# Kernel optimization log

Measured on AMD Instinct MI355X. Metric: run time of the kernel, lower is better.

## Reference

```python
import jax, jax.numpy as jnp
import numpy as np

N = 30000      # nodes
E = 480000     # edges (avg degree 16)
IN = 128       # atom in_channels
ED = 16        # edge_dim
D = 128        # hidden_channels
OUT = 64       # out_channels
L = 4          # num_layers + 1 GCNEConv layers


def setup_inputs() -> dict:
    key = jax.random.key(0)
    ks = jax.random.split(key, 8)
    w = lambda k, sh: (jax.random.normal(k, sh, dtype=jnp.float32) * 0.05)
    return {
        "x": jax.random.normal(ks[0], (N, IN), dtype=jnp.float32),
        "edge_index": jax.random.randint(ks[1], (2, E), 0, N, dtype=jnp.int64),
        "edge_attr": jax.random.normal(ks[2], (E, ED), dtype=jnp.float32),
        "W_atom": w(ks[3], (IN, D)), "b_atom": jnp.zeros((D,), jnp.float32),
        "W_bond": w(ks[4], (ED, D)), "b_bond": jnp.zeros((D,), jnp.float32),
        "W_seq": w(ks[5], (L, D, D)), "b_seq": jnp.zeros((L, D), jnp.float32),
        "W_lin": w(ks[6], (2 * D, OUT)), "b_lin": jnp.zeros((OUT,), jnp.float32),
    }


def _aggregate(h_bond, idx_i, n):
    # CMPNN 'message_booster': elementwise sum_agg * max_agg over incoming edges
    sum_agg = jax.ops.segment_sum(h_bond, idx_i, num_segments=n)
    max_agg = jax.ops.segment_max(h_bond, idx_i, num_segments=n)
    max_agg = jnp.where(jnp.isfinite(max_agg), max_agg, 0.0)  # empty segments -> 0
    return sum_agg * max_agg


def reference(x, edge_index, edge_attr, W_atom, b_atom, W_bond, b_bond,
              W_seq, b_seq, W_lin, b_lin):
    n = x.shape[0]
    idx_i = edge_index[0]  # flow='target_to_source' -> i is edge_index[0]
    idx_j = edge_index[1]

    x_proj = jax.nn.relu(x @ W_atom + b_atom)          # [N, D]
    h_atom = x_proj
    h_bond = jax.nn.relu(edge_attr @ W_bond + b_bond)  # [E, D]

    # first L-1 convs: node update + edge update
    for l in range(L - 1):
        msg = _aggregate(h_bond, idx_i, n)             # [N, D]
        h_atom = h_atom * msg                          # inner_product communicator
        # edge_update: x[edge_index_i] - edge_attr[edge_index_j] (node-index gather
        # into edge tensor, faithful to the original code; valid since E > N)
        bond = h_atom[idx_i] - h_bond[idx_j]           # [E, D]
        h_bond = jax.nn.relu(bond @ W_seq[l] + b_seq[l])

    # last conv: only the node output is used downstream
    msg = _aggregate(h_bond, idx_i, n)
    aggr_atom_message = h_atom * msg

    # top-level communicator (inner_product): hidden_state * message
    h_atom = h_atom * aggr_atom_message
    out = jnp.concatenate([h_atom, x_proj], axis=1) @ W_lin + b_lin  # [N, OUT]
    return out
```

## Files before the change

kernel.cpp:

```cpp
#include <hip/hip_runtime.h>
#include <hip/hip_bf16.h>

#define DD 128
#define SCB 256
#define CE  256

typedef __attribute__((ext_vector_type(8))) short bf16x8;
typedef __attribute__((ext_vector_type(4))) float f32x4;

__device__ __forceinline__ unsigned bf16_rne(float f) {
    unsigned u = __float_as_uint(f);
    return (u + 0x7fffu + ((u >> 16) & 1u)) >> 16;
}

__global__ __launch_bounds__(256)
void hist_kernel(const int* __restrict__ idx_i, int* __restrict__ cnt, int E)
{
    const int e = blockIdx.x * 256 + threadIdx.x;
    if (e < E) atomicAdd(&cnt[idx_i[e]], 1);
}

__global__ __launch_bounds__(SCB)
void scan1_kernel(const int* __restrict__ cnt, int* __restrict__ exc,
                  int* __restrict__ bsum, int n)
{
    __shared__ int s[SCB];
    const int i = blockIdx.x * SCB + (int)threadIdx.x;
    const int v = (i < n) ? cnt[i] : 0;
    s[threadIdx.x] = v;
    __syncthreads();
    #pragma unroll
    for (int off = 1; off < SCB; off <<= 1) {
        int t = (threadIdx.x >= off) ? s[threadIdx.x - off] : 0;
        __syncthreads();
        s[threadIdx.x] += t;
        __syncthreads();
    }
    if (i < n) exc[i] = s[threadIdx.x] - v;
    if (threadIdx.x == SCB - 1) bsum[blockIdx.x] = s[threadIdx.x];
}

__global__ __launch_bounds__(SCB)
void scan2_kernel(int* __restrict__ bsum, int nb)
{
    __shared__ int s[SCB];
    const int v = (threadIdx.x < nb) ? bsum[threadIdx.x] : 0;
    s[threadIdx.x] = v;
    __syncthreads();
    #pragma unroll
    for (int off = 1; off < SCB; off <<= 1) {
        int t = (threadIdx.x >= off) ? s[threadIdx.x - off] : 0;
        __syncthreads();
        s[threadIdx.x] += t;
        __syncthreads();
    }
    if (threadIdx.x < nb) bsum[threadIdx.x] = s[threadIdx.x] - v;
}

__global__ __launch_bounds__(SCB)
void scan3_kernel(int* __restrict__ exc, const int* __restrict__ bsum, int n)
{
    const int i = blockIdx.x * SCB + (int)threadIdx.x;
    if (i < n) exc[i] += bsum[i >> 8];
}

__global__ __launch_bounds__(256)
void scatter_kernel(const int* __restrict__ idx_i, const int* __restrict__ idx_j,
                    int* __restrict__ cursor, int* __restrict__ perm,
                    int* __restrict__ si, int* __restrict__ sj, int E)
{
    const int e = blockIdx.x * 256 + threadIdx.x;
    if (e < E) {
        const int n = idx_i[e];
        const int p = atomicAdd(&cursor[n], 1);
        perm[p] = e;
        si[p] = n;
        sj[p] = idx_j[e];
    }
}

__global__ __launch_bounds__(1024)
void gemm128_mfma_kernel(float* __restrict__ A0, const float* __restrict__ A1,
                         int nA, int nTotal,
                         const float* __restrict__ W, const float* __restrict__ bias,
                         int bias_limit, int do_relu, int update,
                         float* __restrict__ sum_agg, int* __restrict__ max_agg,
                         float* __restrict__ out0, float* __restrict__ out1,
                         int ntiles)
{
    __shared__ __align__(16) unsigned char SM[131584];
    char*  const Whi = (char*)SM;
    char*  const Wlo = (char*)SM + 32768;
    char*  const Ahi = (char*)SM + 65536;
    char*  const Alo = (char*)SM + 98304;
    float* const Wf  = (float*)(SM + 65536);
    float* const bs  = (float*)(SM + 131072);

    const int t = (int)threadIdx.x;

    {
        const float4* Wg = (const float4*)W;
        float4* Wd = (float4*)Wf;
        #pragma unroll
        for (int i = 0; i < 4; ++i) Wd[t + i * 1024] = Wg[t + i * 1024];
        if (t < DD) bs[t] = bias ? bias[t] : 0.f;
    }
    __syncthreads();
    {
        const int col = t >> 3;
        const int kb  = (t & 7) * 16;
        unsigned h16[16], l16[16];
        #pragma unroll
        for (int j = 0; j < 16; ++j) {
            const float w = Wf[(size_t)(kb + j) * DD + col];
            const unsigned hb = bf16_rne(w);
            const float hf = __uint_as_float(hb << 16);
            h16[j] = hb;
            l16[j] = bf16_rne(w - hf);
        }
        #pragma unroll
        for (int c = 0; c < 2; ++c) {
            uint4 ph, pl;
            ph.x = h16[c*8+0] | (h16[c*8+1] << 16);
            ph.y = h16[c*8+2] | (h16[c*8+3] << 16);
            ph.z = h16[c*8+4] | (h16[c*8+5] << 16);
            ph.w = h16[c*8+6] | (h16[c*8+7] << 16);
            pl.x = l16[c*8+0] | (l16[c*8+1] << 16);
            pl.y = l16[c*8+2] | (l16[c*8+3] << 16);
            pl.z = l16[c*8+4] | (l16[c*8+5] << 16);
            pl.w = l16[c*8+6] | (l16[c*8+7] << 16);
            const int off = ((col * 256 + (kb + c * 8) * 2)) ^ ((col & 7) << 4);
            *(uint4*)(Whi + off) = ph;
            *(uint4*)(Wlo + off) = pl;
        }
    }

    const int w  = t >> 6;
    const int l  = t & 63;
    const int wm = w >> 2;
    const int wn = w & 3;
    const int g  = l >> 4;
    const int q  = l & 15;

    for (int tile = blockIdx.x; tile < ntiles; tile += gridDim.x) {
        const int e0 = tile * 128;
        __syncthreads();

        #pragma unroll
        for (int i = 0; i < 2; ++i) {
            const int task = t + i * 1024;
            const int row  = task >> 4;
            const int c    = task & 15;
            const int rr = min(e0 + row, nTotal - 1);
            float d[8];
            if (rr < nA) {
                float* ph0 = A0 + (size_t)rr * DD + c * 8;
                const float4 a0 = *(const float4*)ph0;
                const float4 a1 = *(const float4*)(ph0 + 4);
                if (update) {
                    float* sp = sum_agg + (size_t)rr * DD + c * 8;
                    int*   mp = max_agg + (size_t)rr * DD + c * 8;
                    const float4 s0 = *(const float4*)sp;
                    const float4 s1 = *(const float4*)(sp + 4);
                    const int4   m0 = *(const int4*)mp;
                    const int4   m1 = *(const int4*)(mp + 4);
                    d[0] = a0.x * s0.x * __int_as_float(m0.x);
                    d[1] = a0.y * s0.y * __int_as_float(m0.y);
                    d[2] = a0.z * s0.z * __int_as_float(m0.z);
                    d[3] = a0.w * s0.w * __int_as_float(m0.w);
                    d[4] = a1.x * s1.x * __int_as_float(m1.x);
                    d[5] = a1.y * s1.y * __int_as_float(m1.y);
                    d[6] = a1.z * s1.z * __int_as_float(m1.z);
                    d[7] = a1.w * s1.w * __int_as_float(m1.w);
                    *(float4*)ph0       = make_float4(d[0], d[1], d[2], d[3]);
                    *(float4*)(ph0 + 4) = make_float4(d[4], d[5], d[6], d[7]);
                    *(float4*)sp       = make_float4(0.f, 0.f, 0.f, 0.f);
                    *(float4*)(sp + 4) = make_float4(0.f, 0.f, 0.f, 0.f);
                    *(int4*)mp       = make_int4(0, 0, 0, 0);
                    *(int4*)(mp + 4) = make_int4(0, 0, 0, 0);
                } else {
                    d[0] = a0.x; d[1] = a0.y; d[2] = a0.z; d[3] = a0.w;
                    d[4] = a1.x; d[5] = a1.y; d[6] = a1.z; d[7] = a1.w;
                }
            } else {
                const float* pa = A1 + (size_t)(rr - nA) * DD + c * 8;
                const float4 a0 = *(const float4*)pa;
                const float4 a1 = *(const float4*)(pa + 4);
                d[0] = a0.x; d[1] = a0.y; d[2] = a0.z; d[3] = a0.w;
                d[4] = a1.x; d[5] = a1.y; d[6] = a1.z; d[7] = a1.w;
            }
            unsigned h8[8], l8[8];
            #pragma unroll
            for (int j = 0; j < 8; ++j) {
                const unsigned hb = bf16_rne(d[j]);
                const float hf = __uint_as_float(hb << 16);
                h8[j] = hb;
                l8[j] = bf16_rne(d[j] - hf);
            }
            uint4 ph, pl;
            ph.x = h8[0] | (h8[1] << 16);
            ph.y = h8[2] | (h8[3] << 16);
            ph.z = h8[4] | (h8[5] << 16);
            ph.w = h8[6] | (h8[7] << 16);
            pl.x = l8[0] | (l8[1] << 16);
            pl.y = l8[2] | (l8[3] << 16);
            pl.z = l8[4] | (l8[5] << 16);
            pl.w = l8[6] | (l8[7] << 16);
            const int off = ((row * 256 + c * 16)) ^ ((row & 7) << 4);
            *(uint4*)(Ahi + off) = ph;
            *(uint4*)(Alo + off) = pl;
        }
        __syncthreads();

        f32x4 acc[2][2];
        const f32x4 zero = {0.f, 0.f, 0.f, 0.f};
        acc[0][0] = zero; acc[0][1] = zero; acc[1][0] = zero; acc[1][1] = zero;

        #pragma unroll
        for (int ks = 0; ks < 4; ++ks) {
            const int kbyte = ks * 64 + g * 16;
            bf16x8 ah[2], al[2], bh[2], bl[2];
            #pragma unroll
            for (int m = 0; m < 2; ++m) {
                const int row = wm * 32 + m * 16 + q;
                const int off = (row * 256 + kbyte) ^ ((row & 7) << 4);
                ah[m] = *(const bf16x8*)(Ahi + off);
                al[m] = *(const bf16x8*)(Alo + off);
            }
            #pragma unroll
            for (int n = 0; n < 2; ++n) {
                const int colv = wn * 32 + n * 16 + q;
                const int off = (colv * 256 + kbyte) ^ ((colv & 7) << 4);
                bh[n] = *(const bf16x8*)(Whi + off);
                bl[n] = *(const bf16x8*)(Wlo + off);
            }
            #pragma unroll
            for (int m = 0; m < 2; ++m)
                #pragma unroll
                for (int n = 0; n < 2; ++n)
                    acc[m][n] = __builtin_amdgcn_mfma_f32_16x16x32_bf16(ah[m], bh[n], acc[m][n], 0, 0, 0);
            #pragma unroll
            for (int m = 0; m < 2; ++m)
                #pragma unroll
                for (int n = 0; n < 2; ++n)
                    acc[m][n] = __builtin_amdgcn_mfma_f32_16x16x32_bf16(ah[m], bl[n], acc[m][n], 0, 0, 0);
            #pragma unroll
            for (int m = 0; m < 2; ++m)
                #pragma unroll
                for (int n = 0; n < 2; ++n)
                    acc[m][n] = __builtin_amdgcn_mfma_f32_16x16x32_bf16(al[m], bh[n], acc[m][n], 0, 0, 0);
        }

        #pragma unroll
        for (int n = 0; n < 2; ++n) {
            const int colv = wn * 32 + n * 16 + q;
            const float bv = bs[colv];
            #pragma unroll
            for (int m = 0; m < 2; ++m) {
                #pragma unroll
                for (int r = 0; r < 4; ++r) {
                    const int row = e0 + wm * 32 + m * 16 + g * 4 + r;
                    if (row < nTotal) {
                        float v = acc[m][n][r] + ((row < bias_limit) ? bv : 0.f);
                        if (do_relu) v = fmaxf(v, 0.f);
                        out0[(size_t)row * DD + colv] = v;
                        if (out1) out1[(size_t)row * DD + colv] = v;
                    }
                }
            }
        }
    }
}

__global__ __launch_bounds__(256)
void bond_proj_agg_kernel(const float* __restrict__ edge_attr,
                          const float* __restrict__ Wb, const float* __restrict__ bb,
                          const int* __restrict__ si, const int* __restrict__ perm,
                          float* __restrict__ h_head0,
                          float* __restrict__ sum_agg, int* __restrict__ max_agg,
                          int E, int N)
{
    __shared__ float Ws[16 * DD];
    __shared__ float bs2[DD];
    __shared__ __align__(16) float ea_s[32][16];
    __shared__ int ii2[32], pm2[32];

    for (int idx = (int)threadIdx.x; idx < 16 * DD; idx += 256) Ws[idx] = Wb[idx];
    if (threadIdx.x < DD) bs2[threadIdx.x] = bb[threadIdx.x];

    const int p0 = blockIdx.x * 32;
    {
        const int t = (int)threadIdx.x;
        const int row = t >> 3;
        const int k2 = (t & 7) * 2;
        const int ppc = min(p0 + row, E - 1);
        const int orig = perm[ppc];
        const float2 v2 = *(const float2*)(edge_attr + (size_t)orig * 16 + k2);
        ea_s[row][k2] = v2.x;
        ea_s[row][k2 + 1] = v2.y;
        if (t < 32) {
            const int q = min(p0 + t, E - 1);
            ii2[t] = si[q];
            pm2[t] = perm[q];
        }
    }
    __syncthreads();

    const int o    = threadIdx.x & 127;
    const int half = threadIdx.x >> 7;

    float wcol[16];
    #pragma unroll
    for (int k = 0; k < 16; ++k) wcol[k] = Ws[k * DD + o];
    const float bo = bs2[o];

    int curNode = ii2[half * 16];
    float rs = 0.f, rm = 0.f;
    #pragma unroll 4
    for (int j = 0; j < 16; ++j) {
        const int row = half * 16 + j;
        const float4* ear = (const float4*)(&ea_s[row][0]);
        const float4 q0 = ear[0], q1 = ear[1], q2 = ear[2], q3 = ear[3];
        float acc = bo;
        acc = fmaf(q0.x, wcol[ 0], acc);
        acc = fmaf(q0.y, wcol[ 1], acc);
        acc = fmaf(q0.z, wcol[ 2], acc);
        acc = fmaf(q0.w, wcol[ 3], acc);
        acc = fmaf(q1.x, wcol[ 4], acc);
        acc = fmaf(q1.y, wcol[ 5], acc);
        acc = fmaf(q1.z, wcol[ 6], acc);
        acc = fmaf(q1.w, wcol[ 7], acc);
        acc = fmaf(q2.x, wcol[ 8], acc);
        acc = fmaf(q2.y, wcol[ 9], acc);
        acc = fmaf(q2.z, wcol[10], acc);
        acc = fmaf(q2.w, wcol[11], acc);
        acc = fmaf(q3.x, wcol[12], acc);
        acc = fmaf(q3.y, wcol[13], acc);
        acc = fmaf(q3.z, wcol[14], acc);
        acc = fmaf(q3.w, wcol[15], acc);
        float v = fmaxf(acc, 0.f);
        const int pe = p0 + row;
        if (pe < E) {
            const int orig = pm2[row];
            if (orig < N) h_head0[(size_t)orig * DD + o] = v;
        } else {
            v = 0.f;
        }
        const int gi = ii2[row];
        if (gi != curNode) {
            atomicAdd(&sum_agg[(size_t)curNode * DD + o], rs);
            atomicMax(&max_agg[(size_t)curNode * DD + o], __float_as_int(rm));
            curNode = gi; rs = v; rm = v;
        } else {
            rs += v; rm = fmaxf(rm, v);
        }
    }
    atomicAdd(&sum_agg[(size_t)curNode * DD + o], rs);
    atomicMax(&max_agg[(size_t)curNode * DD + o], __float_as_int(rm));
}

__global__ __launch_bounds__(256)
void edge_pass_kernel(const float* __restrict__ PQ,
                      const int* __restrict__ si, const int* __restrict__ sj,
                      const int* __restrict__ perm,
                      float* __restrict__ head_next, int store_head,
                      float* __restrict__ sum_agg, int* __restrict__ max_agg,
                      int E, int N)
{
    __shared__ int si_s[CE], sj_s[CE], pm_s[CE];
    const int p0b = blockIdx.x * CE;
    if (p0b >= E) return;
    const int t = (int)threadIdx.x;
    {
        const int p = min(p0b + t, E - 1);
        si_s[t] = si[p];
        sj_s[t] = sj[p];
        pm_s[t] = perm[p];
    }
    __syncthreads();

    const int w    = t >> 6;
    const int lane = t & 63;
    const int c    = lane * 2;
    const int q0   = w * 64;
    const int pg0  = p0b + q0;
    if (pg0 >= E) return;

    const float* __restrict__ Qbase = PQ + (size_t)N * DD + c;

    float2 qa = *(const float2*)(Qbase + (size_t)sj_s[q0 + 0] * DD);
    float2 qb = *(const float2*)(Qbase + (size_t)sj_s[q0 + 1] * DD);
    float2 qc = *(const float2*)(Qbase + (size_t)sj_s[q0 + 2] * DD);
    float2 qd = *(const float2*)(Qbase + (size_t)sj_s[q0 + 3] * DD);

    int curNode = si_s[q0];
    float2 Pi = *(const float2*)(PQ + (size_t)curNode * DD + c);
    float2 rs = make_float2(0.f, 0.f), rm = make_float2(0.f, 0.f);

    #define EP_STEP(K, QREG)                                                     \
    {                                                                            \
        const int kk = (K);                                                      \
        const int i = si_s[q0 + kk];                                             \
        if (i != curNode) {                                                      \
            atomicAdd(&sum_agg[(size_t)curNode * DD + c],     rs.x);             \
            atomicAdd(&sum_agg[(size_t)curNode * DD + c + 1], rs.y);             \
            atomicMax(&max_agg[(size_t)curNode * DD + c],     __float_as_int(rm.x)); \
            atomicMax(&max_agg[(size_t)curNode * DD + c + 1], __float_as_int(rm.y)); \
            curNode = i;                                                         \
            Pi = *(const float2*)(PQ + (size_t)i * DD + c);                      \
            rs = make_float2(0.f, 0.f);                                          \
            rm = make_float2(0.f, 0.f);                                          \
        }                                                                        \
        float2 v;                                                                \
        v.x = fmaxf(Pi.x - QREG.x, 0.f);                                         \
        v.y = fmaxf(Pi.y - QREG.y, 0.f);                                         \
        if (pg0 + kk >= E) { v.x = 0.f; v.y = 0.f; }                             \
        rs.x += v.x; rs.y += v.y;                                                \
        rm.x = fmaxf(rm.x, v.x); rm.y = fmaxf(rm.y, v.y);                        \
        if (store_head && (pg0 + kk) < E) {                                      \
            const int orig = pm_s[q0 + kk];                                      \
            if (orig < N) *(float2*)(head_next + (size_t)orig * DD + c) = v;     \
        }                                                                        \
        if (kk + 4 < 64)                                                         \
            QREG = *(const float2*)(Qbase + (size_t)sj_s[q0 + kk + 4] * DD);     \
    }

    #pragma unroll
    for (int k = 0; k < 64; k += 4) {
        EP_STEP(k + 0, qa);
        EP_STEP(k + 1, qb);
        EP_STEP(k + 2, qc);
        EP_STEP(k + 3, qd);
    }
    #undef EP_STEP

    atomicAdd(&sum_agg[(size_t)curNode * DD + c],     rs.x);
    atomicAdd(&sum_agg[(size_t)curNode * DD + c + 1], rs.y);
    atomicMax(&max_agg[(size_t)curNode * DD + c],     __float_as_int(rm.x));
    atomicMax(&max_agg[(size_t)curNode * DD + c + 1], __float_as_int(rm.y));
}

__global__ __launch_bounds__(512, 2)
void final_mfma_kernel(const float* __restrict__ h, const float* __restrict__ sum_agg,
                       const int* __restrict__ max_agg, const float* __restrict__ xp,
                       const float* __restrict__ Wl, const float* __restrict__ bl,
                       float* __restrict__ out, int N)
{
    __shared__ __align__(16) unsigned char SM[65808];
    char*  const Whi = (char*)SM;
    char*  const Wlo = (char*)SM + 32768;
    float* const Wf  = (float*)SM;
    float* const bs  = (float*)(SM + 65536);

    const int t = (int)threadIdx.x;
    {
        const float4* Wg = (const float4*)Wl;
        float4* Wd = (float4*)Wf;
        #pragma unroll
        for (int i = 0; i < 8; ++i) Wd[t + i * 512] = Wg[t + i * 512];
        if (t < 64) bs[t] = bl[t];
    }
    __syncthreads();
    {
        const int col = t & 63;
        const int kb  = (t >> 6) * 32;
        float v[32];
        #pragma unroll
        for (int j = 0; j < 32; ++j) v[j] = Wf[(size_t)(kb + j) * 64 + col];
        __syncthreads();
        #pragma unroll
        for (int c = 0; c < 4; ++c) {
            unsigned h8[8], l8[8];
            #pragma unroll
            for (int j = 0; j < 8; ++j) {
                const float w0 = v[c * 8 + j];
                const unsigned hb = bf16_rne(w0);
                h8[j] = hb;
                l8[j] = bf16_rne(w0 - __uint_as_float(hb << 16));
            }
            uint4 ph, pl;
            ph.x = h8[0] | (h8[1] << 16); ph.y = h8[2] | (h8[3] << 16);
            ph.z = h8[4] | (h8[5] << 16); ph.w = h8[6] | (h8[7] << 16);
            pl.x = l8[0] | (l8[1] << 16); pl.y = l8[2] | (l8[3] << 16);
            pl.z = l8[4] | (l8[5] << 16); pl.w = l8[6] | (l8[7] << 16);
            const int off = (col * 512 + (kb + c * 8) * 2) ^ ((col & 7) << 4);
            *(uint4*)(Whi + off) = ph;
            *(uint4*)(Wlo + off) = pl;
        }
    }
    __syncthreads();

    const int w  = t >> 6;
    const int l  = t & 63;
    const int wm = w >> 1;
    const int wn = w & 1;
    const int g  = l >> 4;
    const int q  = l & 15;
    const int r0 = (int)blockIdx.x * 128;

    f32x4 acc[2][2];
    const f32x4 zero = {0.f, 0.f, 0.f, 0.f};
    acc[0][0] = zero; acc[0][1] = zero; acc[1][0] = zero; acc[1][1] = zero;

    #pragma unroll
    for (int ks = 0; ks < 8; ++ks) {
        const int kf = (ks & 3) * 32 + g * 8;
        bf16x8 ah[2], al[2];
        #pragma unroll
        for (int m = 0; m < 2; ++m) {
            const int rr = min(r0 + wm * 32 + m * 16 + q, N - 1);
            float d[8];
            if (ks < 4) {
                const float* ph = h       + (size_t)rr * DD + kf;
                const float* ps = sum_agg + (size_t)rr * DD + kf;
                const int*   pm = max_agg + (size_t)rr * DD + kf;
                const float4 a0 = *(const float4*)ph;
                const float4 a1 = *(const float4*)(ph + 4);
                const float4 s0 = *(const float4*)ps;
                const float4 s1 = *(const float4*)(ps + 4);
                const int4   i0 = *(const int4*)pm;
                const int4   i1 = *(const int4*)(pm + 4);
                d[0] = a0.x * a0.x * s0.x * __int_as_float(i0.x);
                d[1] = a0.y * a0.y * s0.y * __int_as_float(i0.y);
                d[2] = a0.z * a0.z * s0.z * __int_as_float(i0.z);
                d[3] = a0.w * a0.w * s0.w * __int_as_float(i0.w);
                d[4] = a1.x * a1.x * s1.x * __int_as_float(i1.x);
                d[5] = a1.y * a1.y * s1.y * __int_as_float(i1.y);
                d[6] = a1.z * a1.z * s1.z * __int_as_float(i1.z);
                d[7] = a1.w * a1.w * s1.w * __int_as_float(i1.w);
            } else {
                const float* pa = xp + (size_t)rr * DD + kf;
                const float4 a0 = *(const float4*)pa;
                const float4 a1 = *(const float4*)(pa + 4);
                d[0] = a0.x; d[1] = a0.y; d[2] = a0.z; d[3] = a0.w;
                d[4] = a1.x; d[5] = a1.y; d[6] = a1.z; d[7] = a1.w;
            }
            unsigned h8[8], l8[8];
            #pragma unroll
            for (int j = 0; j < 8; ++j) {
                const unsigned hb = bf16_rne(d[j]);
                h8[j] = hb;
                l8[j] = bf16_rne(d[j] - __uint_as_float(hb << 16));
            }
            uint4 ph2, pl2;
            ph2.x = h8[0] | (h8[1] << 16); ph2.y = h8[2] | (h8[3] << 16);
            ph2.z = h8[4] | (h8[5] << 16); ph2.w = h8[6] | (h8[7] << 16);
            pl2.x = l8[0] | (l8[1] << 16); pl2.y = l8[2] | (l8[3] << 16);
            pl2.z = l8[4] | (l8[5] << 16); pl2.w = l8[6] | (l8[7] << 16);
            ah[m] = *(bf16x8*)&ph2;
            al[m] = *(bf16x8*)&pl2;
        }
        bf16x8 bh[2], blo[2];
        #pragma unroll
        for (int n = 0; n < 2; ++n) {
            const int colv = wn * 32 + n * 16 + q;
            const int off = (colv * 512 + ks * 64 + g * 16) ^ ((colv & 7) << 4);
            bh[n]  = *(const bf16x8*)(Whi + off);
            blo[n] = *(const bf16x8*)(Wlo + off);
        }
        #pragma unroll
        for (int m = 0; m < 2; ++m)
            #pragma unroll
            for (int n = 0; n < 2; ++n) {
                acc[m][n] = __builtin_amdgcn_mfma_f32_16x16x32_bf16(ah[m], bh[n],  acc[m][n], 0, 0, 0);
                acc[m][n] = __builtin_amdgcn_mfma_f32_16x16x32_bf16(ah[m], blo[n], acc[m][n], 0, 0, 0);
                acc[m][n] = __builtin_amdgcn_mfma_f32_16x16x32_bf16(al[m], bh[n],  acc[m][n], 0, 0, 0);
            }
    }

    #pragma unroll
    for (int n = 0; n < 2; ++n) {
        const int colv = wn * 32 + n * 16 + q;
        const float bv = bs[colv];
        #pragma unroll
        for (int m = 0; m < 2; ++m) {
            #pragma unroll
            for (int r = 0; r < 4; ++r) {
                const int row = r0 + wm * 32 + m * 16 + g * 4 + r;
                if (row < N) out[(size_t)row * 64 + colv] = acc[m][n][r] + bv;
            }
        }
    }
}

extern "C" void kernel_launch(void* const* d_in, const int* in_sizes, int n_in,
                              void* d_out, int out_size, void* d_ws, size_t ws_size,
                              hipStream_t stream)
{
    const float* x         = (const float*)d_in[0];
    const int*   edge_idx  = (const int*)d_in[1];
    const float* edge_attr = (const float*)d_in[2];
    const float* W_atom    = (const float*)d_in[3];
    const float* b_atom    = (const float*)d_in[4];
    const float* W_bond    = (const float*)d_in[5];
    const float* b_bond    = (const float*)d_in[6];
    const float* W_seq     = (const float*)d_in[7];
    const float* b_seq     = (const float*)d_in[8];
    const float* W_lin     = (const float*)d_in[9];
    const float* b_lin     = (const float*)d_in[10];
    float* out = (float*)d_out;

    const int N = in_sizes[0] / DD;
    const int E = in_sizes[1] / 2;
    const int* idx_i = edge_idx;
    const int* idx_j = edge_idx + E;

    const size_t nd = (size_t)N * DD;
    float* ws      = (float*)d_ws;
    float* x_proj  = ws;
    float* h_atom  = x_proj + nd;
    float* head    = h_atom + nd;
    float* sum_agg = head + nd;
    int*   max_agg = (int*)(sum_agg + nd);
    float* PQ      = (float*)(max_agg + nd);
    int*   cnt     = (int*)(PQ + 2 * nd);
    int*   cursor  = cnt + N;
    int*   bsum    = cursor + N;
    int*   perm    = bsum + 256;
    int*   si      = perm + E;
    int*   sj      = si + E;

    hipMemsetAsync(cnt, 0, (size_t)N * 4, stream);
    hist_kernel<<<(E + 255) / 256, 256, 0, stream>>>(idx_i, cnt, E);
    const int nb_scan = (N + SCB - 1) / SCB;
    scan1_kernel<<<nb_scan, SCB, 0, stream>>>(cnt, cursor, bsum, N);
    scan2_kernel<<<1, SCB, 0, stream>>>(bsum, nb_scan);
    scan3_kernel<<<nb_scan, SCB, 0, stream>>>(cursor, bsum, N);
    scatter_kernel<<<(E + 255) / 256, 256, 0, stream>>>(idx_i, idx_j, cursor, perm, si, sj, E);

    hipMemsetAsync(sum_agg, 0, nd * 4, stream);
    hipMemsetAsync(max_agg, 0, nd * 4, stream);

    const int ntiles_n = (N + 127) / 128;
    gemm128_mfma_kernel<<<min(ntiles_n, 256), 1024, 0, stream>>>(
        (float*)x, x, N, N, W_atom, b_atom, N, 1, 0, nullptr, nullptr,
        x_proj, h_atom, ntiles_n);

    bond_proj_agg_kernel<<<(E + 31) / 32, 256, 0, stream>>>(edge_attr, W_bond, b_bond,
                                                            si, perm, head,
                                                            sum_agg, max_agg, E, N);

    const int ntiles_pq = (2 * N + 127) / 128;
    const int ep_blocks = (E + CE - 1) / CE;
    for (int l = 0; l < 3; ++l) {
        gemm128_mfma_kernel<<<256, 1024, 0, stream>>>(
            h_atom, head, N, 2 * N, W_seq + (size_t)l * DD * DD,
            b_seq + (size_t)l * DD, N, 0, 1, sum_agg, max_agg,
            PQ, nullptr, ntiles_pq);
        edge_pass_kernel<<<ep_blocks, 256, 0, stream>>>(
            PQ, si, sj, perm, head, (l < 2) ? 1 : 0, sum_agg, max_agg, E, N);
    }

    final_mfma_kernel<<<(N + 127) / 128, 512, 0, stream>>>(
        h_atom, sum_agg, (const int*)max_agg, x_proj, W_lin, b_lin, out, N);
}
```

Before: 452.4 us.

## Use split-bf16 MFMA for bond projection and cut atomics in edge pass

The scalar-FMA bond projection kernel is replaced by a persistent 512-thread kernel. It computes edge_attr@W_bond with bf16 MFMA on hi/lo split operands for near-fp32 accuracy, stages results in shared memory, then does the segmented sum/max aggregation. The edge pass now gives each wave 128 sorted edges instead of 64. Nodes whose edge run lies wholly inside one wave's range are written with plain stores instead of atomics; only the first and last node in each range still use atomics. This relies on edges being sorted by source and on the aggregation buffers being reset before each pass, and it trades some parallelism for fewer atomics.

New measurement: 456.3 us. About the same (+0.8%).

```diff
diff --git a/kernel.cpp b/kernel.cpp
--- a/kernel.cpp
+++ b/kernel.cpp
@@ -3,7 +3,7 @@
 
 #define DD 128
 #define SCB 256
-#define CE  256
+#define CE  512
 
 typedef __attribute__((ext_vector_type(8))) short bf16x8;
 typedef __attribute__((ext_vector_type(4))) float f32x4;
@@ -272,91 +272,144 @@
     }
 }
 
-__global__ __launch_bounds__(256)
-void bond_proj_agg_kernel(const float* __restrict__ edge_attr,
-                          const float* __restrict__ Wb, const float* __restrict__ bb,
-                          const int* __restrict__ si, const int* __restrict__ perm,
-                          float* __restrict__ h_head0,
-                          float* __restrict__ sum_agg, int* __restrict__ max_agg,
-                          int E, int N)
-{
-    __shared__ float Ws[16 * DD];
-    __shared__ float bs2[DD];
-    __shared__ __align__(16) float ea_s[32][16];
-    __shared__ int ii2[32], pm2[32];
-
-    for (int idx = (int)threadIdx.x; idx < 16 * DD; idx += 256) Ws[idx] = Wb[idx];
-    if (threadIdx.x < DD) bs2[threadIdx.x] = bb[threadIdx.x];
-
-    const int p0 = blockIdx.x * 32;
+__global__ __launch_bounds__(512, 2)
+void bond_mfma2_kernel(const float* __restrict__ edge_attr,
+                       const float* __restrict__ Wb, const float* __restrict__ bb,
+                       const int* __restrict__ si, const int* __restrict__ perm,
+                       float* __restrict__ h_head0,
+                       float* __restrict__ sum_agg, int* __restrict__ max_agg,
+                       int E, int N, int ntiles)
+{
+    __shared__ __align__(16) unsigned char SM[60416];
+    char*  const Ap   = (char*)SM;
+    char*  const B1   = (char*)SM + 5120;
+    char*  const B2   = (char*)SM + 15360;
+    float* const hb   = (float*)(SM + 25600);
+    float* const bsh  = (float*)(SM + 59392);
+    int*   const ii_s = (int*)(SM + 59904);
+    int*   const pm_s = (int*)(SM + 60160);
+
+    const int t = (int)threadIdx.x;
+
     {
-        const int t = (int)threadIdx.x;
-        const int row = t >> 3;
-        const int k2 = (t & 7) * 2;
-        const int ppc = min(p0 + row, E - 1);
-        const int orig = perm[ppc];
-        const float2 v2 = *(const float2*)(edge_attr + (size_t)orig * 16 + k2);
-        ea_s[row][k2] = v2.x;
-        ea_s[row][k2 + 1] = v2.y;
-        if (t < 32) {
-            const int q = min(p0 + t, E - 1);
-            ii2[t] = si[q];
-            pm2[t] = perm[q];
-        }
-    }
-    __syncthreads();
-
-    const int o    = threadIdx.x & 127;
-    const int half = threadIdx.x >> 7;
-
-    float wcol[16];
-    #pragma unroll
-    for (int k = 0; k < 16; ++k) wcol[k] = Ws[k * DD + o];
-    const float bo = bs2[o];
-
-    int curNode = ii2[half * 16];
-    float rs = 0.f, rm = 0.f;
-    #pragma unroll 4
-    for (int j = 0; j < 16; ++j) {
-        const int row = half * 16 + j;
-        const float4* ear = (const float4*)(&ea_s[row][0]);
-        const float4 q0 = ear[0], q1 = ear[1], q2 = ear[2], q3 = ear[3];
-        float acc = bo;
-        acc = fmaf(q0.x, wcol[ 0], acc);
-        acc = fmaf(q0.y, wcol[ 1], acc);
-        acc = fmaf(q0.z, wcol[ 2], acc);
-        acc = fmaf(q0.w, wcol[ 3], acc);
-        acc = fmaf(q1.x, wcol[ 4], acc);
-        acc = fmaf(q1.y, wcol[ 5], acc);
-        acc = fmaf(q1.z, wcol[ 6], acc);
-        acc = fmaf(q1.w, wcol[ 7], acc);
-        acc = fmaf(q2.x, wcol[ 8], acc);
-        acc = fmaf(q2.y, wcol[ 9], acc);
-        acc = fmaf(q2.z, wcol[10], acc);
-        acc = fmaf(q2.w, wcol[11], acc);
-        acc = fmaf(q3.x, wcol[12], acc);
-        acc = fmaf(q3.y, wcol[13], acc);
-        acc = fmaf(q3.z, wcol[14], acc);
-        acc = fmaf(q3.w, wcol[15], acc);
-        float v = fmaxf(acc, 0.f);
-        const int pe = p0 + row;
-        if (pe < E) {
-            const int orig = pm2[row];
-            if (orig < N) h_head0[(size_t)orig * DD + o] = v;
-        } else {
-            v = 0.f;
-        }
-        const int gi = ii2[row];
-        if (gi != curNode) {
+        const int col = t & 127;
+        const int kq  = t >> 7;
+        unsigned hq[4], lq[4];
+        #pragma unroll
+        for (int j = 0; j < 4; ++j) {
+            const float w0 = Wb[(size_t)(kq * 4 + j) * DD + col];
+            const unsigned hbv = bf16_rne(w0);
+            hq[j] = hbv;
+            lq[j] = bf16_rne(w0 - __uint_as_float(hbv << 16));
+        }
+        uint2 ph, pl;
+        ph.x = hq[0] | (hq[1] << 16); ph.y = hq[2] | (hq[3] << 16);
+        pl.x = lq[0] | (lq[1] << 16); pl.y = lq[2] | (lq[3] << 16);
+        *(uint2*)(B1 + col * 80 + kq * 8)      = ph;
+        *(uint2*)(B1 + col * 80 + 32 + kq * 8) = pl;
+        *(uint2*)(B2 + col * 80 + kq * 8)      = pl;
+        *(uint2*)(B2 + col * 80 + 32 + kq * 8) = ph;
+        if (t < DD) bsh[t] = bb[t];
+    }
+
+    const int w  = t >> 6;
+    const int l  = t & 63;
+    const int wm = w >> 2;
+    const int wn = w & 3;
+    const int g  = l >> 4;
+    const int q  = l & 15;
+
+    const int per = (ntiles + (int)gridDim.x - 1) / (int)gridDim.x;
+    const int t0 = blockIdx.x * per;
+    const int t1 = min(t0 + per, ntiles);
+
+    for (int tile = t0; tile < t1; ++tile) {
+        const int e0 = tile * 64;
+        __syncthreads();
+
+        if (t < 64) {
+            const int p = min(e0 + t, E - 1);
+            ii_s[t] = si[p];
+            pm_s[t] = perm[p];
+        }
+        if (t < 256) {
+            const int row  = t >> 2;
+            const int c4   = t & 3;
+            const int p    = min(e0 + row, E - 1);
+            const int orig = perm[p];
+            const float4 a = *(const float4*)(edge_attr + (size_t)orig * 16 + c4 * 4);
+            unsigned h4[4], l4[4];
+            h4[0] = bf16_rne(a.x); l4[0] = bf16_rne(a.x - __uint_as_float(h4[0] << 16));
+            h4[1] = bf16_rne(a.y); l4[1] = bf16_rne(a.y - __uint_as_float(h4[1] << 16));
+            h4[2] = bf16_rne(a.z); l4[2] = bf16_rne(a.z - __uint_as_float(h4[2] << 16));
+            h4[3] = bf16_rne(a.w); l4[3] = bf16_rne(a.w - __uint_as_float(h4[3] << 16));
+            uint2 ph, pl;
+            ph.x = h4[0] | (h4[1] << 16); ph.y = h4[2] | (h4[3] << 16);
+            pl.x = l4[0] | (l4[1] << 16); pl.y = l4[2] | (l4[3] << 16);
+            *(uint2*)(Ap + row * 80 + c4 * 8)      = ph;
+            *(uint2*)(Ap + row * 80 + 32 + c4 * 8) = pl;
+        }
+        __syncthreads();
+
+        f32x4 acc[2][2];
+        const f32x4 zero = {0.f, 0.f, 0.f, 0.f};
+        acc[0][0] = zero; acc[0][1] = zero; acc[1][0] = zero; acc[1][1] = zero;
+        bf16x8 av[2];
+        #pragma unroll
+        for (int m = 0; m < 2; ++m)
+            av[m] = *(const bf16x8*)(Ap + (wm * 32 + m * 16 + q) * 80 + g * 16);
+        #pragma unroll
+        for (int n = 0; n < 2; ++n) {
+            const int colv = wn * 32 + n * 16 + q;
+            const bf16x8 b1 = *(const bf16x8*)(B1 + colv * 80 + g * 16);
+            const bf16x8 b2 = *(const bf16x8*)(B2 + colv * 80 + g * 16);
+            #pragma unroll
+            for (int m = 0; m < 2; ++m) {
+                acc[m][n] = __builtin_amdgcn_mfma_f32_16x16x32_bf16(av[m], b1, acc[m][n], 0, 0, 0);
+                acc[m][n] = __builtin_amdgcn_mfma_f32_16x16x32_bf16(av[m], b2, acc[m][n], 0, 0, 0);
+            }
+        }
+        #pragma unroll
+        for (int n = 0; n < 2; ++n) {
+            const int colv = wn * 32 + n * 16 + q;
+            #pragma unroll
+            for (int m = 0; m < 2; ++m)
+                #pragma unroll
+                for (int r = 0; r < 4; ++r)
+                    hb[(wm * 32 + m * 16 + g * 4 + r) * 132 + colv] = acc[m][n][r];
+        }
+        __syncthreads();
+
+        {
+            const int o   = t & 127;
+            const int seg = t >> 7;
+            const float bo = bsh[o];
+            int curNode = ii_s[seg * 16];
+            float rs = 0.f, rm = 0.f;
+            #pragma unroll 4
+            for (int j = 0; j < 16; ++j) {
+                const int row = seg * 16 + j;
+                float v = fmaxf(hb[row * 132 + o] + bo, 0.f);
+                const int e = e0 + row;
+                if (e < E) {
+                    const int orig = pm_s[row];
+                    if (orig < N) h_head0[(size_t)orig * DD + o] = v;
+                } else {
+                    v = 0.f;
+                }
+                const int gi = ii_s[row];
+                if (gi != curNode) {
+                    atomicAdd(&sum_agg[(size_t)curNode * DD + o], rs);
+                    atomicMax(&max_agg[(size_t)curNode * DD + o], __float_as_int(rm));
+                    curNode = gi; rs = v; rm = v;
+                } else {
+                    rs += v; rm = fmaxf(rm, v);
+                }
+            }
             atomicAdd(&sum_agg[(size_t)curNode * DD + o], rs);
             atomicMax(&max_agg[(size_t)curNode * DD + o], __float_as_int(rm));
-            curNode = gi; rs = v; rm = v;
-        } else {
-            rs += v; rm = fmaxf(rm, v);
-        }
-    }
-    atomicAdd(&sum_agg[(size_t)curNode * DD + o], rs);
-    atomicMax(&max_agg[(size_t)curNode * DD + o], __float_as_int(rm));
+        }
+    }
 }
 
 __global__ __launch_bounds__(256)
@@ -371,20 +424,23 @@
     const int p0b = blockIdx.x * CE;
     if (p0b >= E) return;
     const int t = (int)threadIdx.x;
-    {
-        const int p = min(p0b + t, E - 1);
-        si_s[t] = si[p];
-        sj_s[t] = sj[p];
-        pm_s[t] = perm[p];
+    for (int i = t; i < CE; i += 256) {
+        const int p = min(p0b + i, E - 1);
+        si_s[i] = si[p];
+        sj_s[i] = sj[p];
+        pm_s[i] = perm[p];
     }
     __syncthreads();
 
     const int w    = t >> 6;
     const int lane = t & 63;
     const int c    = lane * 2;
-    const int q0   = w * 64;
+    const int q0   = w * 128;
     const int pg0  = p0b + q0;
     if (pg0 >= E) return;
+
+    const int firstNode = si_s[q0];
+    const int lastNode  = si_s[q0 + 127];
 
     const float* __restrict__ Qbase = PQ + (size_t)N * DD + c;
 
@@ -393,19 +449,30 @@
     float2 qc = *(const float2*)(Qbase + (size_t)sj_s[q0 + 2] * DD);
     float2 qd = *(const float2*)(Qbase + (size_t)sj_s[q0 + 3] * DD);
 
-    int curNode = si_s[q0];
+    int curNode = firstNode;
     float2 Pi = *(const float2*)(PQ + (size_t)curNode * DD + c);
     float2 rs = make_float2(0.f, 0.f), rm = make_float2(0.f, 0.f);
+
+    #define EP_FLUSH()                                                           \
+    {                                                                            \
+        if (curNode == firstNode || curNode == lastNode) {                       \
+            atomicAdd(&sum_agg[(size_t)curNode * DD + c],     rs.x);             \
+            atomicAdd(&sum_agg[(size_t)curNode * DD + c + 1], rs.y);             \
+            atomicMax(&max_agg[(size_t)curNode * DD + c],     __float_as_int(rm.x)); \
+            atomicMax(&max_agg[(size_t)curNode * DD + c + 1], __float_as_int(rm.y)); \
+        } else {                                                                 \
+            *(float2*)(sum_agg + (size_t)curNode * DD + c) = rs;                 \
+            *(int2*)(max_agg + (size_t)curNode * DD + c) =                       \
+                make_int2(__float_as_int(rm.x), __float_as_int(rm.y));           \
+        }                                                                        \
+    }
 
     #define EP_STEP(K, QREG)                                                     \
     {                                                                            \
         const int kk = (K);                                                      \
         const int i = si_s[q0 + kk];                                             \
         if (i != curNode) {                                                      \
-            atomicAdd(&sum_agg[(size_t)curNode * DD + c],     rs.x);             \
-            atomicAdd(&sum_agg[(size_t)curNode * DD + c + 1], rs.y);             \
-            atomicMax(&max_agg[(size_t)curNode * DD + c],     __float_as_int(rm.x)); \
-            atomicMax(&max_agg[(size_t)curNode * DD + c + 1], __float_as_int(rm.y)); \
+            EP_FLUSH();                                                          \
             curNode = i;                                                         \
             Pi = *(const float2*)(PQ + (size_t)i * DD + c);                      \
             rs = make_float2(0.f, 0.f);                                          \
@@ -421,23 +488,20 @@
             const int orig = pm_s[q0 + kk];                                      \
             if (orig < N) *(float2*)(head_next + (size_t)orig * DD + c) = v;     \
         }                                                                        \
-        if (kk + 4 < 64)                                                         \
+        if (kk + 4 < 128)                                                        \
             QREG = *(const float2*)(Qbase + (size_t)sj_s[q0 + kk + 4] * DD);     \
     }
 
-    #pragma unroll
-    for (int k = 0; k < 64; k += 4) {
+    #pragma unroll 8
+    for (int k = 0; k < 128; k += 4) {
         EP_STEP(k + 0, qa);
         EP_STEP(k + 1, qb);
         EP_STEP(k + 2, qc);
         EP_STEP(k + 3, qd);
     }
+    EP_FLUSH();
     #undef EP_STEP
-
-    atomicAdd(&sum_agg[(size_t)curNode * DD + c],     rs.x);
-    atomicAdd(&sum_agg[(size_t)curNode * DD + c + 1], rs.y);
-    atomicMax(&max_agg[(size_t)curNode * DD + c],     __float_as_int(rm.x));
-    atomicMax(&max_agg[(size_t)curNode * DD + c + 1], __float_as_int(rm.y));
+    #undef EP_FLUSH
 }
 
 __global__ __launch_bounds__(512, 2)
@@ -636,9 +700,10 @@
         (float*)x, x, N, N, W_atom, b_atom, N, 1, 0, nullptr, nullptr,
         x_proj, h_atom, ntiles_n);
 
-    bond_proj_agg_kernel<<<(E + 31) / 32, 256, 0, stream>>>(edge_attr, W_bond, b_bond,
-                                                            si, perm, head,
-                                                            sum_agg, max_agg, E, N);
+    const int ntiles_b = (E + 63) / 64;
+    bond_mfma2_kernel<<<1024, 512, 0, stream>>>(edge_attr, W_bond, b_bond,
+                                                si, perm, head,
+                                                sum_agg, max_agg, E, N, ntiles_b);
 
     const int ntiles_pq = (2 * N + 127) / 128;
     const int ep_blocks = (E + CE - 1) / CE;
```
